# Optimization experiments

Measured on AMD Instinct MI355X. Metric: run time of the kernel, lower is better.

Reference implementation:

```python
import jax, jax.numpy as jnp
import numpy as np

N = 100000      # nodes
E = 800000      # edges
D = 96          # feature dim (feats_per_node == layer_1_feats == layer_2_feats)
NEG_SLOPE = 0.01  # torch.nn.LeakyReLU default


def setup_inputs() -> dict:
    key = jax.random.key(0)
    kx, ks, kd, k1, k2, k3, k4 = jax.random.split(key, 7)
    # ensure every node appears at least once as a source row so e_rowsum > 0
    src = jnp.concatenate([jnp.arange(N, dtype=jnp.int64),
                           jax.random.randint(ks, (E - N,), 0, N, dtype=jnp.int64)])
    dst = jax.random.randint(kd, (E,), 0, N, dtype=jnp.int64)
    edge_index = jnp.stack([src, dst])  # [2, E]
    x = jax.random.normal(kx, (N, D), dtype=jnp.float32)
    # xavier-normal-like params, scaled down to keep exp() well-behaved
    W1 = jax.random.normal(k1, (D, D), dtype=jnp.float32) * 0.1
    a1 = jax.random.normal(k2, (1, 2 * D), dtype=jnp.float32) * 0.1
    W2 = jax.random.normal(k3, (D, D), dtype=jnp.float32) * 0.1
    a2 = jax.random.normal(k4, (1, 2 * D), dtype=jnp.float32) * 0.1
    return {"edge_index": edge_index, "x": x, "W1": W1, "a1": a1, "W2": W2, "a2": a2}


def _gat_layer(h_in, W, a, src, dst):
    h = h_in @ W                                   # [N, D]
    d = h.shape[1]
    # a @ cat(h[src], h[dst]) without materializing the concat:
    s = h[src] @ a[0, :d] + h[dst] @ a[0, d:]      # [E]
    e = jnp.exp(-jax.nn.leaky_relu(s, NEG_SLOPE))  # [E]
    n = h.shape[0]
    rowsum = jax.ops.segment_sum(e, src, num_segments=n)               # spmm(edge, e, ones)
    h_prime = jax.ops.segment_sum(e[:, None] * h[dst], src, num_segments=n)  # spmm(edge, e, h)
    return h_prime / rowsum[:, None]


def reference(edge_index, x, W1, a1, W2, a2):
    src, dst = edge_index[0], edge_index[1]
    h = _gat_layer(x, W1, a1, src, dst)
    h = _gat_layer(h, W2, a2, src, dst)
    return jax.nn.relu(h)
```

## Files before the change

kernel.cpp:

```cpp
#include <hip/hip_runtime.h>
#include <hip/hip_bf16.h>

#define NN 100000
#define NE 800000
#define DIM 96
#define NEG_SLOPE 0.01f
#define PAD 48
#define SCAN_BLOCKS ((NN + 255) / 256)
#define EDGE_BLOCKS ((NE + 255) / 256)
#define CONV_BLOCKS ((2 * DIM * DIM + 255) / 256)
#define GEMM_GRID   ((NN + 63) / 64)
#define AGG_BLOCKS  ((NN / 2 + 3) / 4)

typedef short bf16x8 __attribute__((ext_vector_type(8)));
typedef float f32x4  __attribute__((ext_vector_type(4)));
typedef float f32x2  __attribute__((ext_vector_type(2)));

__device__ __forceinline__ unsigned short f32_to_bf16_rne(float f) {
    unsigned int u = __float_as_uint(f);
    unsigned int r = (u + 0x7FFFu + ((u >> 16) & 1u)) >> 16;
    return (unsigned short)r;
}
__device__ __forceinline__ float bf16lo_to_f32(unsigned int u) { return __uint_as_float(u << 16); }
__device__ __forceinline__ float bf16hi_to_f32(unsigned int u) { return __uint_as_float(u & 0xFFFF0000u); }

__device__ __forceinline__ int   rdlane_i(int v, int l)   { return __builtin_amdgcn_readlane(v, l); }
__device__ __forceinline__ float rdlane_f(float v, int l) {
    return __uint_as_float((unsigned int)__builtin_amdgcn_readlane((int)__float_as_uint(v), l));
}


__global__ __launch_bounds__(256) void prep_kernel(int* __restrict__ cnt,
                                                   const float* __restrict__ W1, unsigned short* __restrict__ Wt1,
                                                   const float* __restrict__ W2, unsigned short* __restrict__ Wt2) {
    if (blockIdx.x < CONV_BLOCKS) {
        int idx = blockIdx.x * 256 + threadIdx.x;
        if (idx < DIM * DIM) {
            int n = idx / DIM, k = idx % DIM;
            Wt1[n * DIM + k] = f32_to_bf16_rne(W1[k * DIM + n]);
        } else if (idx < 2 * DIM * DIM) {
            int j = idx - DIM * DIM;
            int n = j / DIM, k = j % DIM;
            Wt2[n * DIM + k] = f32_to_bf16_rne(W2[k * DIM + n]);
        }
    } else {
        int i = (blockIdx.x - CONV_BLOCKS) * 256 + threadIdx.x;
        if (i < NN) cnt[i] = 0;
    }
}


template <bool A_BF16>
__device__ __forceinline__ void gemm_body(int bid, const void* __restrict__ A_,
                                          const unsigned short* __restrict__ Wt,
                                          const float* __restrict__ avec,
                                          unsigned short* __restrict__ Hout,
                                          float* __restrict__ ssrc, float* __restrict__ sdst,
                                          int n) {
    const int wave = threadIdx.x >> 6;
    const int lane = threadIdx.x & 63;
    const int quad = lane >> 4;
    const int l16  = lane & 15;
    const int R0   = bid * 64 + wave * 16;

    bf16x8 bfr[6][3];
#pragma unroll
    for (int nt = 0; nt < 6; nt++) {
        const unsigned short* wrow = Wt + (size_t)(nt * 16 + l16) * DIM;
#pragma unroll
        for (int kc = 0; kc < 3; kc++) bfr[nt][kc] = *(const bf16x8*)(wrow + kc * 32 + quad * 8);
    }

    int arow = R0 + l16;
    if (arow >= n) arow = n - 1;
    bf16x8 afr[3];
    if (A_BF16) {
        const unsigned short* ap = (const unsigned short*)A_ + (size_t)arow * DIM;
#pragma unroll
        for (int kc = 0; kc < 3; kc++) afr[kc] = *(const bf16x8*)(ap + kc * 32 + quad * 8);
    } else {
        const float* ap = (const float*)A_ + (size_t)arow * DIM;
#pragma unroll
        for (int kc = 0; kc < 3; kc++) {
            float4 lo = *(const float4*)(ap + kc * 32 + quad * 8);
            float4 hi = *(const float4*)(ap + kc * 32 + quad * 8 + 4);
            union { bf16x8 v; unsigned short u[8]; } t;
            t.u[0] = f32_to_bf16_rne(lo.x); t.u[1] = f32_to_bf16_rne(lo.y);
            t.u[2] = f32_to_bf16_rne(lo.z); t.u[3] = f32_to_bf16_rne(lo.w);
            t.u[4] = f32_to_bf16_rne(hi.x); t.u[5] = f32_to_bf16_rne(hi.y);
            t.u[6] = f32_to_bf16_rne(hi.z); t.u[7] = f32_to_bf16_rne(hi.w);
            afr[kc] = t.v;
        }
    }

    f32x4 acc[6];
#pragma unroll
    for (int nt = 0; nt < 6; nt++) acc[nt] = (f32x4){0.f, 0.f, 0.f, 0.f};
#pragma unroll
    for (int kc = 0; kc < 3; kc++)
#pragma unroll
        for (int nt = 0; nt < 6; nt++)
            acc[nt] = __builtin_amdgcn_mfma_f32_16x16x32_bf16(afr[kc], bfr[nt][kc], acc[nt], 0, 0, 0);

    float as_[6], ad_[6];
#pragma unroll
    for (int nt = 0; nt < 6; nt++) {
        as_[nt] = avec[nt * 16 + l16];
        ad_[nt] = avec[96 + nt * 16 + l16];
    }
    float ps[4], pd[4];
#pragma unroll
    for (int r = 0; r < 4; r++) {
        float s = 0.f, d = 0.f;
#pragma unroll
        for (int nt = 0; nt < 6; nt++) {
            s = fmaf(acc[nt][r], as_[nt], s);
            d = fmaf(acc[nt][r], ad_[nt], d);
        }
        ps[r] = s; pd[r] = d;
    }
#pragma unroll
    for (int m = 1; m < 16; m <<= 1) {
#pragma unroll
        for (int r = 0; r < 4; r++) {
            ps[r] += __shfl_xor(ps[r], m);
            pd[r] += __shfl_xor(pd[r], m);
        }
    }
    {
        float psel = (l16 == 0) ? ps[0] : (l16 == 1) ? ps[1] : (l16 == 2) ? ps[2] : ps[3];
        float dsel = (l16 == 8) ? pd[0] : (l16 == 9) ? pd[1] : (l16 == 10) ? pd[2] : pd[3];
        int rs = R0 + quad * 4 + l16;
        int rd = R0 + quad * 4 + (l16 - 8);
        if (l16 < 4 && rs < n) ssrc[rs] = psel;
        if (l16 >= 8 && l16 < 12 && rd < n) sdst[rd] = dsel;
    }

#pragma unroll
    for (int r = 0; r < 4; r++) {
        int orow = R0 + quad * 4 + r;
        if (orow < n) {
            unsigned short* hrow = Hout + (size_t)orow * DIM;
#pragma unroll
            for (int nt = 0; nt < 6; nt++) hrow[nt * 16 + l16] = f32_to_bf16_rne(acc[nt][r]);
        }
    }
}

template <bool A_BF16>
__global__ __launch_bounds__(256) void gemm_mfma_kernel(const void* __restrict__ A_,
                                                        const unsigned short* __restrict__ Wt,
                                                        const float* __restrict__ avec,
                                                        unsigned short* __restrict__ Hout,
                                                        float* __restrict__ ssrc, float* __restrict__ sdst,
                                                        int n) {
    gemm_body<A_BF16>(blockIdx.x, A_, Wt, avec, Hout, ssrc, sdst, n);
}


__global__ __launch_bounds__(256) void gemm1_scatter_kernel(const float* __restrict__ x,
                                                            const unsigned short* __restrict__ Wt1,
                                                            const float* __restrict__ a1,
                                                            unsigned short* __restrict__ h1,
                                                            float* __restrict__ ssrc, float* __restrict__ sdst,
                                                            const int* __restrict__ src, const int* __restrict__ dst,
                                                            int* __restrict__ cnt, int* __restrict__ temp) {
    if (blockIdx.x < GEMM_GRID) {
        gemm_body<false>(blockIdx.x, x, Wt1, a1, h1, ssrc, sdst, NN);
    } else {
        int e = (blockIdx.x - GEMM_GRID) * 256 + threadIdx.x;
        if (e < NE) {
            int s = src[e];
            int r = atomicAdd(&cnt[s], 1);
            r = min(r, PAD - 1);
            temp[(size_t)s * PAD + r] = dst[e];
        }
    }
}


template <bool RELU, bool OUT_BF16>
__global__ __launch_bounds__(256) void agg_kernel(const unsigned short* __restrict__ h,
                                                  const float* __restrict__ ssrc,
                                                  const float* __restrict__ sdst,
                                                  const int* __restrict__ cnt,
                                                  const int* __restrict__ temp,
                                                  void* __restrict__ out) {
    int gid  = blockIdx.x * 256 + threadIdx.x;
    int wid  = gid >> 6;
    int lane = threadIdx.x & 63;
    int n0   = wid * 2;
    if (n0 >= NN) return;
    int n1 = n0 + 1;

    int c0 = min(cnt[n0], PAD);
    int c1 = min(cnt[n1], PAD);
    const int* t0 = temp + (size_t)n0 * PAD;
    const int* t1 = temp + (size_t)n1 * PAD;
    float ss = ssrc[n0 + ((lane >> 3) & 1)];
    const bool act = lane < 48;
    const int  li8 = lane & 7;

    float a00 = 0.f, a01 = 0.f, w0 = 0.f;
    float a10 = 0.f, a11 = 0.f, w1 = 0.f;

    const int cmax = max(c0, c1);
    for (int p = 0; p < cmax; p += 8) {
        const int r0 = c0 - p;
        const int r1 = c1 - p;
        int dv = (lane < 8) ? t0[min(p + lane, c0 - 1)] : t1[min(p + li8, c1 - 1)];

        bool valid = (lane < 8) ? (lane < r0) : ((lane < 16) && (li8 < r1));
        float sv = 0.f;
        if (valid) sv = sdst[dv];

        unsigned int u0[8], u1[8];
#pragma unroll
        for (int i = 0; i < 8; i++) {
            int d0i = rdlane_i(dv, i);
            int d1i = rdlane_i(dv, 8 + i);
            if (act) {
                u0[i] = ((const unsigned int*)(h + (size_t)d0i * DIM))[lane];
                u1[i] = ((const unsigned int*)(h + (size_t)d1i * DIM))[lane];
            }
        }

        float wl = 0.f;
        if (valid) {
            float s  = ss + sv;
            float lr = s > 0.f ? s : NEG_SLOPE * s;
            wl = __expf(-lr);
        }

#pragma unroll
        for (int i = 0; i < 8; i++) {
            float wa = rdlane_f(wl, i);
            float wb = rdlane_f(wl, 8 + i);
            w0 += wa; w1 += wb;
            if (act) {
                a00 = fmaf(wa, bf16lo_to_f32(u0[i]), a00);
                a01 = fmaf(wa, bf16hi_to_f32(u0[i]), a01);
                a10 = fmaf(wb, bf16lo_to_f32(u1[i]), a10);
                a11 = fmaf(wb, bf16hi_to_f32(u1[i]), a11);
            }
        }
    }

    float inv0 = 1.f / w0;
    float inv1 = 1.f / w1;
    float r00 = a00 * inv0, r01 = a01 * inv0;
    float r10 = a10 * inv1, r11 = a11 * inv1;
    if (RELU) {
        r00 = fmaxf(r00, 0.f); r01 = fmaxf(r01, 0.f);
        r10 = fmaxf(r10, 0.f); r11 = fmaxf(r11, 0.f);
    }
    if (act) {
        if (OUT_BF16) {
            unsigned int pk0 = (unsigned int)f32_to_bf16_rne(r00) | ((unsigned int)f32_to_bf16_rne(r01) << 16);
            unsigned int pk1 = (unsigned int)f32_to_bf16_rne(r10) | ((unsigned int)f32_to_bf16_rne(r11) << 16);
            ((unsigned int*)out)[(size_t)n0 * 48 + lane] = pk0;
            ((unsigned int*)out)[(size_t)n1 * 48 + lane] = pk1;
        } else {
            f32x2 v0; v0.x = r00; v0.y = r01;
            f32x2 v1; v1.x = r10; v1.y = r11;
            __builtin_nontemporal_store(v0, &((f32x2*)out)[(size_t)n0 * 48 + lane]);
            __builtin_nontemporal_store(v1, &((f32x2*)out)[(size_t)n1 * 48 + lane]);
        }
    }
}


extern "C" void kernel_launch(void* const* d_in, const int* in_sizes, int n_in,
                              void* d_out, int out_size, void* d_ws, size_t ws_size,
                              hipStream_t stream) {
    (void)in_sizes; (void)n_in; (void)out_size; (void)ws_size;
    const int*   edge_index = (const int*)d_in[0];
    const float* x  = (const float*)d_in[1];
    const float* W1 = (const float*)d_in[2];
    const float* a1 = (const float*)d_in[3];
    const float* W2 = (const float*)d_in[4];
    const float* a2 = (const float*)d_in[5];
    float* out = (float*)d_out;

    const int* src = edge_index;
    const int* dst = edge_index + NE;

    char* ws = (char*)d_ws;
    size_t off = 0;
    auto alloc = [&](size_t bytes) -> void* {
        void* p = ws + off;
        off += (bytes + 255) & ~(size_t)255;
        return p;
    };
    unsigned short* h1 = (unsigned short*)alloc((size_t)NN * DIM * 2);
    unsigned short* h2 = (unsigned short*)alloc((size_t)NN * DIM * 2);
    int*   temp      = (int*)alloc((size_t)NN * PAD * 4);
    float* ssrc      = (float*)alloc((size_t)NN * 4);
    float* sdst      = (float*)alloc((size_t)NN * 4);
    int*   cnt       = (int*)alloc((size_t)NN * 4);
    unsigned short* Wt1 = (unsigned short*)alloc((size_t)DIM * DIM * 2);
    unsigned short* Wt2 = (unsigned short*)alloc((size_t)DIM * DIM * 2);

    prep_kernel<<<CONV_BLOCKS + SCAN_BLOCKS, 256, 0, stream>>>(cnt, W1, Wt1, W2, Wt2);

    gemm1_scatter_kernel<<<GEMM_GRID + EDGE_BLOCKS, 256, 0, stream>>>(x, Wt1, a1, h1, ssrc, sdst,
                                                                     src, dst, cnt, temp);
    agg_kernel<false, true><<<AGG_BLOCKS, 256, 0, stream>>>(h1, ssrc, sdst, cnt, temp, h2);

    gemm_mfma_kernel<true><<<GEMM_GRID, 256, 0, stream>>>(h2, Wt2, a2, h1, ssrc, sdst, NN);
    agg_kernel<true, false><<<AGG_BLOCKS, 256, 0, stream>>>(h1, ssrc, sdst, cnt, temp, out);
}
```

Before: 228.2 us.

## Fuse layer-1 aggregation with layer-2 GEMM via LDS-staged MFMA tile

Adds a kernel in which each block aggregates 8 nodes for layer 1, stages the bf16 rows in LDS, and has one wave compute the layer-2 projection and attention scores with MFMA. This removes one launch and the global write and read of the intermediate h2. The edge-scatter blocks are also moved ahead of the GEMM blocks in the first kernel so they get scheduled earlier. The cost is that only one of four waves does the GEMM while the other three sit idle, and the MFMA tile is half-filled because only 8 of its 16 rows are used. Separate ssrc2/sdst2 buffers are added so the fused kernel does not overwrite scores that other blocks are still reading.

```diff
diff --git a/kernel.cpp b/kernel.cpp
--- a/kernel.cpp
+++ b/kernel.cpp
@@ -11,6 +11,7 @@
 #define CONV_BLOCKS ((2 * DIM * DIM + 255) / 256)
 #define GEMM_GRID   ((NN + 63) / 64)
 #define AGG_BLOCKS  ((NN / 2 + 3) / 4)
+#define AGG1_BLOCKS (NN / 8)
 
 typedef short bf16x8 __attribute__((ext_vector_type(8)));
 typedef float f32x4  __attribute__((ext_vector_type(4)));
@@ -147,16 +148,6 @@
     }
 }
 
-template <bool A_BF16>
-__global__ __launch_bounds__(256) void gemm_mfma_kernel(const void* __restrict__ A_,
-                                                        const unsigned short* __restrict__ Wt,
-                                                        const float* __restrict__ avec,
-                                                        unsigned short* __restrict__ Hout,
-                                                        float* __restrict__ ssrc, float* __restrict__ sdst,
-                                                        int n) {
-    gemm_body<A_BF16>(blockIdx.x, A_, Wt, avec, Hout, ssrc, sdst, n);
-}
-
 
 __global__ __launch_bounds__(256) void gemm1_scatter_kernel(const float* __restrict__ x,
                                                             const unsigned short* __restrict__ Wt1,
@@ -165,15 +156,163 @@
                                                             float* __restrict__ ssrc, float* __restrict__ sdst,
                                                             const int* __restrict__ src, const int* __restrict__ dst,
                                                             int* __restrict__ cnt, int* __restrict__ temp) {
-    if (blockIdx.x < GEMM_GRID) {
-        gemm_body<false>(blockIdx.x, x, Wt1, a1, h1, ssrc, sdst, NN);
-    } else {
-        int e = (blockIdx.x - GEMM_GRID) * 256 + threadIdx.x;
+    if (blockIdx.x < EDGE_BLOCKS) {
+        int e = blockIdx.x * 256 + threadIdx.x;
         if (e < NE) {
             int s = src[e];
             int r = atomicAdd(&cnt[s], 1);
             r = min(r, PAD - 1);
             temp[(size_t)s * PAD + r] = dst[e];
+        }
+    } else {
+        gemm_body<false>(blockIdx.x - EDGE_BLOCKS, x, Wt1, a1, h1, ssrc, sdst, NN);
+    }
+}
+
+
+__global__ __launch_bounds__(256) void agg1_gemm2_kernel(const unsigned short* __restrict__ h,
+                                                         const float* __restrict__ ssrc,
+                                                         const float* __restrict__ sdst,
+                                                         const int* __restrict__ cnt,
+                                                         const int* __restrict__ temp,
+                                                         const unsigned short* __restrict__ Wt2,
+                                                         const float* __restrict__ a2,
+                                                         unsigned short* __restrict__ hL2,
+                                                         float* __restrict__ ssrc2, float* __restrict__ sdst2) {
+    __shared__ unsigned short lds_h[16][104];
+    const int wid  = threadIdx.x >> 6;
+    const int lane = threadIdx.x & 63;
+    const int base = blockIdx.x * 8;
+    const int n0   = base + wid * 2;
+    const int n1   = n0 + 1;
+
+    int c0 = min(cnt[n0], PAD);
+    int c1 = min(cnt[n1], PAD);
+    const int* t0 = temp + (size_t)n0 * PAD;
+    const int* t1 = temp + (size_t)n1 * PAD;
+    float ss = ssrc[n0 + ((lane >> 3) & 1)];
+    const bool act = lane < 48;
+    const int  li8 = lane & 7;
+
+    float a00 = 0.f, a01 = 0.f, w0 = 0.f;
+    float a10 = 0.f, a11 = 0.f, w1 = 0.f;
+
+    const int cmax = max(c0, c1);
+    for (int p = 0; p < cmax; p += 8) {
+        const int r0 = c0 - p;
+        const int r1 = c1 - p;
+        int dv = (lane < 8) ? t0[min(p + lane, c0 - 1)] : t1[min(p + li8, c1 - 1)];
+
+        bool valid = (lane < 8) ? (lane < r0) : ((lane < 16) && (li8 < r1));
+        float sv = 0.f;
+        if (valid) sv = sdst[dv];
+
+        unsigned int u0[8], u1[8];
+#pragma unroll
+        for (int i = 0; i < 8; i++) {
+            int d0i = rdlane_i(dv, i);
+            int d1i = rdlane_i(dv, 8 + i);
+            if (act) {
+                u0[i] = ((const unsigned int*)(h + (size_t)d0i * DIM))[lane];
+                u1[i] = ((const unsigned int*)(h + (size_t)d1i * DIM))[lane];
+            }
+        }
+
+        float wl = 0.f;
+        if (valid) {
+            float s  = ss + sv;
+            float lr = s > 0.f ? s : NEG_SLOPE * s;
+            wl = __expf(-lr);
+        }
+
+#pragma unroll
+        for (int i = 0; i < 8; i++) {
+            float wa = rdlane_f(wl, i);
+            float wb = rdlane_f(wl, 8 + i);
+            w0 += wa; w1 += wb;
+            if (act) {
+                a00 = fmaf(wa, bf16lo_to_f32(u0[i]), a00);
+                a01 = fmaf(wa, bf16hi_to_f32(u0[i]), a01);
+                a10 = fmaf(wb, bf16lo_to_f32(u1[i]), a10);
+                a11 = fmaf(wb, bf16hi_to_f32(u1[i]), a11);
+            }
+        }
+    }
+
+    float inv0 = 1.f / w0;
+    float inv1 = 1.f / w1;
+    float r00 = a00 * inv0, r01 = a01 * inv0;
+    float r10 = a10 * inv1, r11 = a11 * inv1;
+    if (act) {
+        unsigned int pk0 = (unsigned int)f32_to_bf16_rne(r00) | ((unsigned int)f32_to_bf16_rne(r01) << 16);
+        unsigned int pk1 = (unsigned int)f32_to_bf16_rne(r10) | ((unsigned int)f32_to_bf16_rne(r11) << 16);
+        *(unsigned int*)&lds_h[wid * 2 + 0][lane * 2] = pk0;
+        *(unsigned int*)&lds_h[wid * 2 + 1][lane * 2] = pk1;
+    }
+    __syncthreads();
+    if (wid != 0) return;
+
+    const int quad = lane >> 4;
+    const int l16  = lane & 15;
+
+    bf16x8 afr[3];
+#pragma unroll
+    for (int kc = 0; kc < 3; kc++)
+        afr[kc] = *(const bf16x8*)&lds_h[l16][kc * 32 + quad * 8];
+
+    f32x4 acc[6];
+#pragma unroll
+    for (int nt = 0; nt < 6; nt++) acc[nt] = (f32x4){0.f, 0.f, 0.f, 0.f};
+#pragma unroll
+    for (int nt = 0; nt < 6; nt++) {
+        const unsigned short* wrow = Wt2 + (size_t)(nt * 16 + l16) * DIM;
+#pragma unroll
+        for (int kc = 0; kc < 3; kc++) {
+            bf16x8 bfr = *(const bf16x8*)(wrow + kc * 32 + quad * 8);
+            acc[nt] = __builtin_amdgcn_mfma_f32_16x16x32_bf16(afr[kc], bfr, acc[nt], 0, 0, 0);
+        }
+    }
+
+    float as_[6], ad_[6];
+#pragma unroll
+    for (int nt = 0; nt < 6; nt++) {
+        as_[nt] = a2[nt * 16 + l16];
+        ad_[nt] = a2[96 + nt * 16 + l16];
+    }
+    float ps[4], pd[4];
+#pragma unroll
+    for (int r = 0; r < 4; r++) {
+        float s = 0.f, d = 0.f;
+#pragma unroll
+        for (int nt = 0; nt < 6; nt++) {
+            s = fmaf(acc[nt][r], as_[nt], s);
+            d = fmaf(acc[nt][r], ad_[nt], d);
+        }
+        ps[r] = s; pd[r] = d;
+    }
+#pragma unroll
+    for (int m = 1; m < 16; m <<= 1) {
+#pragma unroll
+        for (int r = 0; r < 4; r++) {
+            ps[r] += __shfl_xor(ps[r], m);
+            pd[r] += __shfl_xor(pd[r], m);
+        }
+    }
+    {
+        float psel = (l16 == 0) ? ps[0] : (l16 == 1) ? ps[1] : (l16 == 2) ? ps[2] : ps[3];
+        float dsel = (l16 == 8) ? pd[0] : (l16 == 9) ? pd[1] : (l16 == 10) ? pd[2] : pd[3];
+        int rls = quad * 4 + l16;
+        int rld = quad * 4 + (l16 - 8);
+        if (l16 < 4 && rls < 8) ssrc2[base + rls] = psel;
+        if (l16 >= 8 && l16 < 12 && rld < 8) sdst2[base + rld] = dsel;
+    }
+#pragma unroll
+    for (int r = 0; r < 4; r++) {
+        int rl = quad * 4 + r;
+        if (rl < 8) {
+            unsigned short* hrow = hL2 + (size_t)(base + rl) * DIM;
+#pragma unroll
+            for (int nt = 0; nt < 6; nt++) hrow[nt * 16 + l16] = f32_to_bf16_rne(acc[nt][r]);
         }
     }
 }
@@ -292,21 +431,24 @@
         off += (bytes + 255) & ~(size_t)255;
         return p;
     };
-    unsigned short* h1 = (unsigned short*)alloc((size_t)NN * DIM * 2);
-    unsigned short* h2 = (unsigned short*)alloc((size_t)NN * DIM * 2);
+    unsigned short* h1  = (unsigned short*)alloc((size_t)NN * DIM * 2);
+    unsigned short* hL2 = (unsigned short*)alloc((size_t)NN * DIM * 2);
     int*   temp      = (int*)alloc((size_t)NN * PAD * 4);
     float* ssrc      = (float*)alloc((size_t)NN * 4);
     float* sdst      = (float*)alloc((size_t)NN * 4);
+    float* ssrc2     = (float*)alloc((size_t)NN * 4);
+    float* sdst2     = (float*)alloc((size_t)NN * 4);
     int*   cnt       = (int*)alloc((size_t)NN * 4);
     unsigned short* Wt1 = (unsigned short*)alloc((size_t)DIM * DIM * 2);
     unsigned short* Wt2 = (unsigned short*)alloc((size_t)DIM * DIM * 2);
 
     prep_kernel<<<CONV_BLOCKS + SCAN_BLOCKS, 256, 0, stream>>>(cnt, W1, Wt1, W2, Wt2);
 
-    gemm1_scatter_kernel<<<GEMM_GRID + EDGE_BLOCKS, 256, 0, stream>>>(x, Wt1, a1, h1, ssrc, sdst,
+    gemm1_scatter_kernel<<<EDGE_BLOCKS + GEMM_GRID, 256, 0, stream>>>(x, Wt1, a1, h1, ssrc, sdst,
                                                                      src, dst, cnt, temp);
-    agg_kernel<false, true><<<AGG_BLOCKS, 256, 0, stream>>>(h1, ssrc, sdst, cnt, temp, h2);
-
-    gemm_mfma_kernel<true><<<GEMM_GRID, 256, 0, stream>>>(h2, Wt2, a2, h1, ssrc, sdst, NN);
-    agg_kernel<true, false><<<AGG_BLOCKS, 256, 0, stream>>>(h1, ssrc, sdst, cnt, temp, out);
-}
+
+    agg1_gemm2_kernel<<<AGG1_BLOCKS, 256, 0, stream>>>(h1, ssrc, sdst, cnt, temp,
+                                                       Wt2, a2, hL2, ssrc2, sdst2);
+
+    agg_kernel<true, false><<<AGG_BLOCKS, 256, 0, stream>>>(hL2, ssrc2, sdst2, cnt, temp, out);
+}
```

Result: slower. 242.0 us (+6.0%).
